# Kernel tuning notes

Hardware: AMD Instinct MI355X
Metric: run time of the kernel (lower is better)

## Reference

```python
import jax, jax.numpy as jnp
import numpy as np

K = 3        # kernel size
PAD = 1      # padding
DG = 16      # deformable groups
MAXR = 10.0  # max_residue_magnitude


def _lrelu(x):
    return jnp.where(x >= 0, x, 0.1 * x)


def _conv3(x, w, b):
    y = jax.lax.conv_general_dilated(x, w, (1, 1), 'SAME',
                                     dimension_numbers=('NCHW', 'OIHW', 'NCHW'))
    return y + b[None, :, None, None]


def _deform_conv2d(x, offset, mask, weight, bias):
    # x: [B,Cin,H,W]; offset: [B,2*DG*K*K,H,W]; mask: [B,DG*K*K,H,W]
    B, Cin, H, W = x.shape
    Cout = weight.shape[0]
    G, Cg, K2 = DG, Cin // DG, K * K
    off = offset.reshape(B, G, K2, 2, H, W)
    dy, dx = off[:, :, :, 0], off[:, :, :, 1]
    ky = jnp.repeat(jnp.arange(K), K).astype(x.dtype)   # [K2]
    kx = jnp.tile(jnp.arange(K), K).astype(x.dtype)
    hh = jnp.arange(H, dtype=x.dtype)
    ww = jnp.arange(W, dtype=x.dtype)
    # sampling positions [B,G,K2,H,W]
    py = dy + ky[None, None, :, None, None] + hh[None, None, None, :, None] - PAD
    px = dx + kx[None, None, :, None, None] + ww[None, None, None, None, :] - PAD
    y0 = jnp.floor(py)
    x0 = jnp.floor(px)
    wy1 = py - y0
    wx1 = px - x0
    xf = x.reshape(B, G, Cg, H * W)

    def gather(yi, xi, wgt):
        valid = (yi >= 0) & (yi <= H - 1) & (xi >= 0) & (xi <= W - 1)
        idx = (jnp.clip(yi, 0, H - 1).astype(jnp.int32) * W
               + jnp.clip(xi, 0, W - 1).astype(jnp.int32)).reshape(B, G, -1)
        vals = jnp.take_along_axis(
            xf, jnp.broadcast_to(idx[:, :, None, :], (B, G, Cg, idx.shape[-1])), axis=3)
        vals = vals.reshape(B, G, Cg, K2, H, W)
        w = (wgt * valid.astype(x.dtype))[:, :, None]  # [B,G,1,K2,H,W]
        return vals * w

    s = (gather(y0, x0, (1 - wy1) * (1 - wx1))
         + gather(y0, x0 + 1, (1 - wy1) * wx1)
         + gather(y0 + 1, x0, wy1 * (1 - wx1))
         + gather(y0 + 1, x0 + 1, wy1 * wx1))
    s = s * mask.reshape(B, G, K2, H, W)[:, :, None]
    wr = weight.reshape(Cout, G, Cg, K2)
    out = jnp.einsum('ogck,bgckhw->bohw', wr, s)
    return out + bias[None, :, None, None]


def setup_inputs() -> dict:
    key = jax.random.key(0)
    ks = jax.random.split(key, 16)
    B, Cin, Cout, H, W = 4, 128, 64, 96, 96
    Coff = 3 * Cout + 4  # 196
    stdv = 1.0 / np.sqrt(Cin * K * K)
    inp = {
        'x': jax.random.normal(ks[0], (B, Cin, H, W), jnp.float32),
        'extra_feat': jax.random.normal(ks[1], (B, 3 * Cout, H, W), jnp.float32),
        'flow_1': jax.random.normal(ks[2], (B, 2, H, W), jnp.float32),
        'flow_2': jax.random.normal(ks[3], (B, 2, H, W), jnp.float32),
        'weight': jax.random.uniform(ks[4], (Cout, Cin, K, K), jnp.float32, -stdv, stdv),
        'bias': jax.random.normal(ks[5], (Cout,), jnp.float32) * 0.01,
        'ow0': jax.random.normal(ks[6], (Cout, Coff, K, K), jnp.float32) * 0.02,
        'ob0': jnp.zeros((Cout,), jnp.float32),
        'ow1': jax.random.normal(ks[7], (Cout, Cout, K, K), jnp.float32) * 0.02,
        'ob1': jnp.zeros((Cout,), jnp.float32),
        'ow2': jax.random.normal(ks[8], (Cout, Cout, K, K), jnp.float32) * 0.02,
        'ob2': jnp.zeros((Cout,), jnp.float32),
        'ow3': jax.random.normal(ks[9], (27 * DG, Cout, K, K), jnp.float32) * 0.01,
        'ob3': jnp.zeros((27 * DG,), jnp.float32),
    }
    return inp


def reference(x, extra_feat, flow_1, flow_2, weight, bias,
              ow0, ob0, ow1, ob1, ow2, ob2, ow3, ob3):
    feat = jnp.concatenate([extra_feat, flow_1, flow_2], axis=1)
    h = _lrelu(_conv3(feat, ow0, ob0))
    h = _lrelu(_conv3(h, ow1, ob1))
    h = _lrelu(_conv3(h, ow2, ob2))
    out = _conv3(h, ow3, ob3)
    o1, o2, m = jnp.split(out, 3, axis=1)
    offs = MAXR * jnp.tanh(jnp.concatenate([o1, o2], axis=1))
    off1, off2 = jnp.split(offs, 2, axis=1)
    off1 = off1 + jnp.tile(flow_1[:, ::-1], (1, off1.shape[1] // 2, 1, 1))
    off2 = off2 + jnp.tile(flow_2[:, ::-1], (1, off2.shape[1] // 2, 1, 1))
    offset = jnp.concatenate([off1, off2], axis=1)
    mask = jax.nn.sigmoid(m)
    return _deform_conv2d(x, offset, mask, weight, bias)
```

## Files before the change

kernel.cpp:

```cpp
#include <hip/hip_runtime.h>
#include <math.h>

#define HW 9216
#define Hh 96
#define Ww 96
#define PHW 9604
#define QSLOTS 9604

typedef __attribute__((ext_vector_type(8))) short bh8;
typedef __attribute__((ext_vector_type(4))) short bh4;
typedef __attribute__((ext_vector_type(4))) float f32x4;
typedef __attribute__((ext_vector_type(2))) float f32x2;
typedef __attribute__((ext_vector_type(4))) int i32x4;
union bh8i { bh8 v; i32x4 i; };

__device__ __forceinline__ short f2bf(float f) {
    union { float f; unsigned u; } v; v.f = f;
    unsigned r = v.u + 0x7FFFu + ((v.u >> 16) & 1u);
    return (short)(r >> 16);
}
__device__ __forceinline__ float bf2f(short s) {
    union { unsigned u; float f; } v; v.u = ((unsigned)(unsigned short)s) << 16;
    return v.f;
}
__device__ __forceinline__ float lo_bf(unsigned u) {
    union { unsigned u; float f; } v; v.u = u << 16; return v.f;
}
__device__ __forceinline__ float hi_bf(unsigned u) {
    union { unsigned u; float f; } v; v.u = u & 0xFFFF0000u; return v.f;
}
__device__ __forceinline__ int cvt_pk_bf16(float lo, float hi) {
    int r;
    asm("v_cvt_pk_bf16_f32 %0, %1, %2" : "=v"(r) : "v"(lo), "v"(hi));
    return r;
}

__global__ void prep_misc(short* __restrict__ xpad1, short* __restrict__ hpa,
                          short* __restrict__ hpb, short* __restrict__ xdp,
                          const float* __restrict__ ow0, const float* __restrict__ ow1,
                          const float* __restrict__ ow2, const float* __restrict__ ow3,
                          const float* __restrict__ wd,
                          short* __restrict__ wb0, short* __restrict__ wb1,
                          short* __restrict__ wb2, short* __restrict__ wb3,
                          short* __restrict__ wbd) {
    int i = blockIdx.x * 256 + threadIdx.x;
    const int z1 = 4 * 388 * 224, z2 = 4 * 388 * 64;
    if (i < z1 + 2 * z2) {
        short* p; int C;
        if (i < z1) { p = xpad1; C = 224; }
        else if (i < z1 + z2) { p = hpa; C = 64; i -= z1; }
        else { p = hpb; C = 64; i -= z1 + z2; }
        int c = i % C;
        int r = i / C;
        int b = r / 388, pid = r - b * 388;
        int row, col;
        if (pid < 98)       { row = 0;  col = pid; }
        else if (pid < 196) { row = 97; col = pid - 98; }
        else if (pid < 292) { row = pid - 196 + 1; col = 0; }
        else                { row = pid - 292 + 1; col = 97; }
        p[((size_t)b * PHW + row * 98 + col) * C + c] = 0;
        return;
    }
    i -= z1 + 2 * z2;
    const int zr = 64 * 579 * 4;
    if (i < zr) {
        int piece = i & 3;
        int r2 = i >> 2;
        int s = r2 % 579, bg = r2 / 579;
        int y, x;
        if (s < 98)       { y = 0;  x = s; }
        else if (s < 196) { y = 96; x = s - 98; }
        else if (s < 294) { y = 97; x = s - 196; }
        else {
            int s2 = s - 294;
            int xi = s2 / 95;
            x = (xi == 0) ? 0 : ((xi == 1) ? 96 : 97);
            y = 1 + s2 - xi * 95;
        }
        *(bh8*)&xdp[(((size_t)bg * QSLOTS) + y * 98 + x) * 32 + piece * 8] =
            (bh8){0, 0, 0, 0, 0, 0, 0, 0};
        return;
    }
    i -= zr;
    const int n0 = 64 * 9 * 224, n1 = 64 * 9 * 64, n3 = 448 * 9 * 64, nd = 144 * 64 * 8;
    if (i < n0) {
        int co = i / (9 * 224); int r = i - co * (9 * 224);
        int tap = r / 224, ci = r - tap * 224;
        wb0[i] = f2bf(ci < 196 ? ow0[(co * 196 + ci) * 9 + tap] : 0.f);
        return;
    }
    i -= n0;
    if (i < n1) {
        int co = i / (9 * 64); int r = i - co * (9 * 64);
        int tap = r / 64, ci = r - tap * 64;
        wb1[i] = f2bf(ow1[(co * 64 + ci) * 9 + tap]);
        return;
    }
    i -= n1;
    if (i < n1) {
        int co = i / (9 * 64); int r = i - co * (9 * 64);
        int tap = r / 64, ci = r - tap * 64;
        wb2[i] = f2bf(ow2[(co * 64 + ci) * 9 + tap]);
        return;
    }
    i -= n1;
    if (i < n3) {
        int co = i / (9 * 64); int r = i - co * (9 * 64);
        int tap = r / 64, ci = r - tap * 64;
        wb3[i] = f2bf(co < 432 ? ow3[(co * 64 + ci) * 9 + tap] : 0.f);
        return;
    }
    i -= n3;
    if (i < nd) {
        int gt = i >> 9, r = i & 511;
        int co = r >> 3, c = r & 7;
        int g = gt / 9, tap = gt - g * 9;
        wbd[i] = f2bf(wd[(co * 128 + g * 8 + c) * 9 + tap]);
    }
}

__global__ void pack_all(const float* __restrict__ extra,
                         const float* __restrict__ f1,
                         const float* __restrict__ f2,
                         const float* __restrict__ x,
                         short* __restrict__ xp,
                         short* __restrict__ xdp) {
    __shared__ float t[32][33];
    const int tid = threadIdx.x, tx = tid & 31, ty = tid >> 5;
    const int pt = blockIdx.x, b = blockIdx.z;
    if (blockIdx.y < 7) {
        const int ct = blockIdx.y;
#pragma unroll
        for (int j = 0; j < 4; ++j) {
            int ch = ct * 32 + ty + j * 8;
            int p = pt * 32 + tx;
            float v = 0.f;
            if (ch < 192)      v = extra[(b * 192 + ch) * HW + p];
            else if (ch < 194) v = f1[(b * 2 + ch - 192) * HW + p];
            else if (ch < 196) v = f2[(b * 2 + ch - 194) * HW + p];
            t[ty + j * 8][tx] = v;
        }
        __syncthreads();
#pragma unroll
        for (int j = 0; j < 4; ++j) {
            int pr = ty + j * 8;
            int p = pt * 32 + pr;
            int r = p / 96, c = p - r * 96;
            xp[((size_t)b * PHW + (r + 1) * 98 + (c + 1)) * 224 + ct * 32 + tx] =
                f2bf(t[tx][pr]);
        }
    } else {
        const int ct = blockIdx.y - 7;
#pragma unroll
        for (int j = 0; j < 4; ++j) {
            int ch = ct * 32 + ty + j * 8;
            t[ty + j * 8][tx] = x[((size_t)b * 128 + ch) * HW + pt * 32 + tx];
        }
        __syncthreads();
        if (tid < 128) {
            int oct = tid >> 5, p = tid & 31;
            int g = ct * 4 + oct;
            int pix = pt * 32 + p;
            int r = pix / 96, c = pix - r * 96;
            bh8 v;
#pragma unroll
            for (int cc = 0; cc < 8; ++cc) v[cc] = f2bf(t[oct * 8 + cc][p]);
            size_t sb = ((size_t)b * 16 + g) * QSLOTS;
            int pr = r + 1, pc = c + 1;
            *(bh8*)&xdp[(sb + pr * 98 + pc) * 32 + 0]        = v;
            *(bh8*)&xdp[(sb + pr * 98 + pc - 1) * 32 + 8]    = v;
            *(bh8*)&xdp[(sb + (pr - 1) * 98 + pc) * 32 + 16] = v;
            *(bh8*)&xdp[(sb + (pr - 1) * 98 + pc - 1) * 32 + 24] = v;
        }
    }
}

template<int CINP, int KCH>
__launch_bounds__(256)
__global__ void conv_mfma(const short* __restrict__ xp,
                          const short* __restrict__ wb,
                          const float* __restrict__ bias,
                          short* __restrict__ o1) {
    __shared__ __attribute__((aligned(16))) short smA[9 * 64 * 32];
    const int tid = threadIdx.x;
    const int lane = tid & 63, wv = tid >> 6;
    const int q = lane >> 4, l15 = lane & 15;
    const int b = blockIdx.y;
    const int pix0 = blockIdx.x * 64 + wv * 16;
    const int soh = pix0 / 96, sow = pix0 - (pix0 / 96) * 96;

    const short* bp = xp + ((size_t)b * PHW + soh * 98 + sow + l15) * CINP + q * 8;

    const int sco = tid >> 2, sqq = tid & 3;
    const short* wsrc = wb + (size_t)sco * (9 * CINP) + sqq * 8;

    f32x4 acc[4];
#pragma unroll
    for (int t = 0; t < 4; ++t) acc[t] = (f32x4){0.f, 0.f, 0.f, 0.f};

    for (int p = 0; p < KCH; ++p) {
        __syncthreads();
        bh8 wtmp[9];
#pragma unroll
        for (int tap = 0; tap < 9; ++tap)
            wtmp[tap] = *(const bh8*)(wsrc + tap * CINP + p * 32);
#pragma unroll
        for (int tap = 0; tap < 9; ++tap)
            *(bh8*)&smA[tap * 2048 + sco * 32 + sqq * 8] = wtmp[tap];
        __syncthreads();
#pragma unroll
        for (int tap = 0; tap < 9; ++tap) {
            const int ky = tap / 3, kx = tap - (tap / 3) * 3;
            bh8 bf = *(const bh8*)(bp + (ky * 98 + kx) * CINP + p * 32);
#pragma unroll
            for (int t = 0; t < 4; ++t) {
                bh8 af = *(const bh8*)&smA[tap * 2048 + (t * 16 + l15) * 32 + q * 8];
                acc[t] = __builtin_amdgcn_mfma_f32_16x16x32_bf16(af, bf, acc[t], 0, 0, 0);
            }
        }
    }

    size_t base = ((size_t)b * PHW + (soh + 1) * 98 + sow + l15 + 1) * 64;
#pragma unroll
    for (int t = 0; t < 4; ++t) {
        bh4 v4;
#pragma unroll
        for (int r = 0; r < 4; ++r) {
            int co = t * 16 + q * 4 + r;
            float v = acc[t][r] + bias[co];
            v = (v >= 0.f) ? v : 0.1f * v;
            v4[r] = f2bf(v);
        }
        *(bh4*)(o1 + base + t * 16 + q * 4) = v4;
    }
}

__launch_bounds__(256)
__global__ void conv4_gemm(const short* __restrict__ xp,
                           const short* __restrict__ wb,
                           const float* __restrict__ bias,
                           float* __restrict__ offp,
                           short* __restrict__ maskb,
                           const float* __restrict__ flow1,
                           const float* __restrict__ flow2) {
    __shared__ __attribute__((aligned(16))) short smA[64 * 64];
    __shared__ __attribute__((aligned(16))) short smB[192 * 64];
    const int tid = threadIdx.x;
    const int lane = tid & 63, wv = tid >> 6;
    const int q = lane >> 4, l15 = lane & 15;
    const int pg = blockIdx.x;
    const int b = blockIdx.y;
    const int cob = blockIdx.z * 64;
    const int r0 = pg * 2;

    f32x4 acc[3][4];
#pragma unroll
    for (int pf = 0; pf < 3; ++pf)
#pragma unroll
        for (int cf = 0; cf < 4; ++cf) acc[pf][cf] = (f32x4){0.f, 0.f, 0.f, 0.f};

    for (int tap = 0; tap < 9; ++tap) {
        const int ky = tap / 3, kx = tap - (tap / 3) * 3;
        __syncthreads();
#pragma unroll
        for (int it = 0; it < 2; ++it) {
            int id = it * 256 + tid;
            int row = id >> 3, s = id & 7;
            int sw = s ^ (row & 7);
            *(bh8*)&smA[row * 64 + sw * 8] =
                *(const bh8*)(wb + (size_t)(cob + row) * 576 + tap * 64 + s * 8);
        }
#pragma unroll
        for (int it = 0; it < 6; ++it) {
            int id = it * 256 + tid;
            int row = id >> 3, s = id & 7;
            int sw = s ^ (row & 7);
            int srow = (row >= 96) ? 1 : 0;
            int scol = row - srow * 96;
            *(bh8*)&smB[row * 64 + sw * 8] = *(const bh8*)&xp[
                ((size_t)b * PHW + (r0 + srow + ky) * 98 + scol + kx) * 64 + s * 8];
        }
        __syncthreads();
#pragma unroll
        for (int kc = 0; kc < 2; ++kc) {
            bh8 bf[3], af[4];
#pragma unroll
            for (int pf = 0; pf < 3; ++pf) {
                int row = wv * 48 + pf * 16 + l15;
                int sw = (kc * 4 + q) ^ (row & 7);
                bf[pf] = *(const bh8*)&smB[row * 64 + sw * 8];
            }
#pragma unroll
            for (int cf = 0; cf < 4; ++cf) {
                int row = cf * 16 + l15;
                int sw = (kc * 4 + q) ^ (row & 7);
                af[cf] = *(const bh8*)&smA[row * 64 + sw * 8];
            }
#pragma unroll
            for (int pf = 0; pf < 3; ++pf)
#pragma unroll
                for (int cf = 0; cf < 4; ++cf)
                    acc[pf][cf] = __builtin_amdgcn_mfma_f32_16x16x32_bf16(
                        af[cf], bf[pf], acc[pf][cf], 0, 0, 0);
        }
    }

#pragma unroll
    for (int pf = 0; pf < 3; ++pf) {
        int local = wv * 48 + pf * 16 + l15;
        int lrow = (local >= 96) ? 1 : 0;
        int pix = (r0 + lrow) * 96 + (local - lrow * 96);
#pragma unroll
        for (int cf = 0; cf < 4; ++cf) {
            int cb0 = cob + cf * 16 + q * 4;
            if (cb0 < 288) {
                const float* fl = (cb0 < 144) ? flow1 : flow2;
                float fe = fl[(b * 2 + 1) * HW + pix];
                float fo = fl[(b * 2) * HW + pix];
                float t0 = 10.f * tanhf(acc[pf][cf][0] + bias[cb0 + 0]) + fe;
                float t1 = 10.f * tanhf(acc[pf][cf][1] + bias[cb0 + 1]) + fo;
                float t2 = 10.f * tanhf(acc[pf][cf][2] + bias[cb0 + 2]) + fe;
                float t3 = 10.f * tanhf(acc[pf][cf][3] + bias[cb0 + 3]) + fo;
                size_t p0 = ((size_t)b * 144 + (cb0 >> 1)) * HW + pix;
                *(f32x2*)&offp[p0 * 2] = (f32x2){t0, t1};
                *(f32x2*)&offp[(p0 + HW) * 2] = (f32x2){t2, t3};
            } else {
#pragma unroll
                for (int r = 0; r < 4; ++r) {
                    int chn = cb0 + r;
                    if (chn < 432) {
                        float v = acc[pf][cf][r] + bias[chn];
                        maskb[((size_t)b * 144 + (chn - 288)) * HW + pix] =
                            f2bf(1.f / (1.f + expf(-v)));
                    }
                }
            }
        }
    }
}

__launch_bounds__(256)
__global__ void deform_mfma(const short* __restrict__ xdp,
                            const float* __restrict__ offp,
                            const short* __restrict__ maskb,
                            const short* __restrict__ wbd,
                            const float* __restrict__ bias,
                            float* __restrict__ out) {
    __shared__ float red[4][1024];
    const int tid = threadIdx.x;
    const int lane = tid & 63, wv = tid >> 6;
    const int q = lane >> 4, l15 = lane & 15;
    const int blk = blockIdx.x;
    const int xs = blk & 7, idx = blk >> 3;
    const int b = xs >> 1;
    const int pix0 = ((xs & 1) * 288 + idx) * 16;
    const int pix = pix0 + l15;
    const int h = pix / 96, w = pix - (pix / 96) * 96;

    const short* xb = xdp + (size_t)b * 16 * QSLOTS * 32;

    f32x4 acc[4];
#pragma unroll
    for (int t = 0; t < 4; ++t) acc[t] = (f32x4){0.f, 0.f, 0.f, 0.f};

#pragma unroll
    for (int chunk = 0; chunk < 4; ++chunk) {
        const int g = wv * 4 + chunk;
        const float* opp = offp + (((size_t)b * 144 + g * 9) * HW + pix) * 2;
        const short* mp  = maskb + ((size_t)b * 144 + g * 9) * HW + pix;

        f32x2 dxy[9];
        float mk[9];
#pragma unroll
        for (int i = 0; i < 9; ++i) {
            dxy[i] = *(const f32x2*)(opp + (size_t)i * HW * 2);
            mk[i]  = bf2f(mp[(size_t)i * HW]);
        }

        int soff[9];
        float wq[9];
#pragma unroll
        for (int i = 0; i < 9; ++i) {
            float py = dxy[i][0] + (float)(i / 3) + (float)h - 1.f;
            float px = dxy[i][1] + (float)(i % 3) + (float)w - 1.f;
            py = fminf(fmaxf(py, -1.f), 96.f);
            px = fminf(fmaxf(px, -1.f), 96.f);
            float y0f = floorf(py), x0f = floorf(px);
            float wy1 = py - y0f, wx1 = px - x0f;
            int yp = (int)y0f + 1, xp = (int)x0f + 1;
            soff[i] = ((g * QSLOTS + yp * 98 + xp) << 5) + q * 8;
            float wy = (q & 2) ? wy1 : (1.f - wy1);
            float wx = (q & 1) ? wx1 : (1.f - wx1);
            wq[i] = wy * wx * mk[i];
        }

#pragma unroll
        for (int i = 0; i < 9; ++i) {
            bh8i cv;
            cv.v = *(const bh8*)(xb + soff[i]);
            const f32x2 w2 = (f32x2){wq[i], wq[i]};
            bh8i bf;
#pragma unroll
            for (int k2 = 0; k2 < 4; ++k2) {
                unsigned u = (unsigned)cv.i[k2];
                f32x2 pv = (f32x2){lo_bf(u), hi_bf(u)} * w2;
                bf.i[k2] = cvt_pk_bf16(pv[0], pv[1]);
            }
            const int gt = g * 9 + i;
            const short* ap = wbd + ((size_t)gt * 64 + l15) * 8;
#pragma unroll
            for (int t = 0; t < 4; ++t) {
                bh8 af = *(const bh8*)(ap + t * 128);
                acc[t] = __builtin_amdgcn_mfma_f32_16x16x32_bf16(af, bf.v, acc[t], 0, 0, 0);
            }
        }
    }

#pragma unroll
    for (int t = 0; t < 4; ++t)
#pragma unroll
        for (int r = 0; r < 4; ++r)
            red[wv][(t * 16 + q * 4 + r) * 16 + l15] = acc[t][r];
    __syncthreads();
    for (int e = tid; e < 1024; e += 256) {
        int co = e >> 4, pl = e & 15;
        float v = red[0][e] + red[1][e] + red[2][e] + red[3][e] + bias[co];
        out[((size_t)b * 64 + co) * HW + pix0 + pl] = v;
    }
}

extern "C" void kernel_launch(void* const* d_in, const int* in_sizes, int n_in,
                              void* d_out, int out_size, void* d_ws, size_t ws_size,
                              hipStream_t stream) {
    const float* x      = (const float*)d_in[0];
    const float* extra  = (const float*)d_in[1];
    const float* flow1  = (const float*)d_in[2];
    const float* flow2  = (const float*)d_in[3];
    const float* weight = (const float*)d_in[4];
    const float* bias   = (const float*)d_in[5];
    const float* ow0    = (const float*)d_in[6];
    const float* ob0    = (const float*)d_in[7];
    const float* ow1    = (const float*)d_in[8];
    const float* ob1    = (const float*)d_in[9];
    const float* ow2    = (const float*)d_in[10];
    const float* ob2    = (const float*)d_in[11];
    const float* ow3    = (const float*)d_in[12];
    const float* ob3    = (const float*)d_in[13];
    float* out = (float*)d_out;

    char* wsb = (char*)d_ws;
    short* xpad1 = (short*)wsb;   wsb += (size_t)4 * PHW * 224 * 2;
    short* hpa   = (short*)wsb;   wsb += (size_t)4 * PHW * 64 * 2;
    short* hpb   = (short*)wsb;   wsb += (size_t)4 * PHW * 64 * 2;
    float* offpair = (float*)wsb; wsb += (size_t)4 * 144 * HW * 2 * 4;
    short* maskbuf = (short*)wsb; wsb += (size_t)4 * 144 * HW * 2;
    short* xdp     = (short*)wsb; wsb += (size_t)4 * 16 * QSLOTS * 32 * 2 + 64;
    short* wb0     = (short*)wsb; wsb += 64 * 9 * 224 * 2;
    short* wb1     = (short*)wsb; wsb += 64 * 9 * 64 * 2;
    short* wb2     = (short*)wsb; wsb += 64 * 9 * 64 * 2;
    short* wb3     = (short*)wsb; wsb += 448 * 9 * 64 * 2;
    short* wbd     = (short*)wsb;

    const int prep_total = 546304 + 148224 + 534528;
    prep_misc<<<dim3((prep_total + 255) / 256), 256, 0, stream>>>(
        xpad1, hpa, hpb, xdp, ow0, ow1, ow2, ow3, weight,
        wb0, wb1, wb2, wb3, wbd);
    pack_all<<<dim3(288, 11, 4), 256, 0, stream>>>(extra, flow1, flow2, x, xpad1, xdp);

    conv_mfma<224, 7><<<dim3(144, 4), 256, 0, stream>>>(xpad1, wb0, ob0, hpa);
    conv_mfma<64, 2><<<dim3(144, 4), 256, 0, stream>>>(hpa, wb1, ob1, hpb);
    conv_mfma<64, 2><<<dim3(144, 4), 256, 0, stream>>>(hpb, wb2, ob2, hpa);
    conv4_gemm<<<dim3(48, 4, 7), 256, 0, stream>>>(hpa, wb3, ob3, offpair,
                                                   maskbuf, flow1, flow2);
    deform_mfma<<<dim3(2304), 256, 0, stream>>>(xdp, offpair, maskbuf, wbd, bias, out);
}
```

Measured before the change: 314.3 us.

## Restructure final offset conv to stage all-tap weights and read activations directly

The last conv (64->432 channels) now keeps all 9 taps of a 64x32 weight slice in shared memory and loads activation fragments straight from global memory per wave, instead of staging both operands per tap in LDS. Each block covers 64 pixels instead of 192, so the grid triples and there are fewer barriers per block. This cuts shared-memory traffic and synchronisation but drops activation reuse across output-channel tiles within a block, relying on cache for the repeated input reads.

Result: slower. 325.7 us (+3.6%).

```diff
diff --git a/kernel.cpp b/kernel.cpp
--- a/kernel.cpp
+++ b/kernel.cpp
@@ -236,103 +236,76 @@
 }
 
 __launch_bounds__(256)
-__global__ void conv4_gemm(const short* __restrict__ xp,
+__global__ void conv4_mfma(const short* __restrict__ xp,
                            const short* __restrict__ wb,
                            const float* __restrict__ bias,
                            float* __restrict__ offp,
                            short* __restrict__ maskb,
                            const float* __restrict__ flow1,
                            const float* __restrict__ flow2) {
-    __shared__ __attribute__((aligned(16))) short smA[64 * 64];
-    __shared__ __attribute__((aligned(16))) short smB[192 * 64];
+    __shared__ __attribute__((aligned(16))) short smA[9 * 64 * 32];
     const int tid = threadIdx.x;
     const int lane = tid & 63, wv = tid >> 6;
     const int q = lane >> 4, l15 = lane & 15;
-    const int pg = blockIdx.x;
     const int b = blockIdx.y;
     const int cob = blockIdx.z * 64;
-    const int r0 = pg * 2;
-
-    f32x4 acc[3][4];
-#pragma unroll
-    for (int pf = 0; pf < 3; ++pf)
-#pragma unroll
-        for (int cf = 0; cf < 4; ++cf) acc[pf][cf] = (f32x4){0.f, 0.f, 0.f, 0.f};
-
-    for (int tap = 0; tap < 9; ++tap) {
-        const int ky = tap / 3, kx = tap - (tap / 3) * 3;
-        __syncthreads();
-#pragma unroll
-        for (int it = 0; it < 2; ++it) {
-            int id = it * 256 + tid;
-            int row = id >> 3, s = id & 7;
-            int sw = s ^ (row & 7);
-            *(bh8*)&smA[row * 64 + sw * 8] =
-                *(const bh8*)(wb + (size_t)(cob + row) * 576 + tap * 64 + s * 8);
-        }
-#pragma unroll
-        for (int it = 0; it < 6; ++it) {
-            int id = it * 256 + tid;
-            int row = id >> 3, s = id & 7;
-            int sw = s ^ (row & 7);
-            int srow = (row >= 96) ? 1 : 0;
-            int scol = row - srow * 96;
-            *(bh8*)&smB[row * 64 + sw * 8] = *(const bh8*)&xp[
-                ((size_t)b * PHW + (r0 + srow + ky) * 98 + scol + kx) * 64 + s * 8];
-        }
-        __syncthreads();
-#pragma unroll
-        for (int kc = 0; kc < 2; ++kc) {
-            bh8 bf[3], af[4];
-#pragma unroll
-            for (int pf = 0; pf < 3; ++pf) {
-                int row = wv * 48 + pf * 16 + l15;
-                int sw = (kc * 4 + q) ^ (row & 7);
-                bf[pf] = *(const bh8*)&smB[row * 64 + sw * 8];
+    const int pix0 = blockIdx.x * 64 + wv * 16;
+    const int soh = pix0 / 96, sow = pix0 - (pix0 / 96) * 96;
+
+    const short* bp = xp + ((size_t)b * PHW + soh * 98 + sow + l15) * 64 + q * 8;
+
+    const int sco = tid >> 2, sqq = tid & 3;
+    const short* wsrc = wb + (size_t)(cob + sco) * 576 + sqq * 8;
+
+    f32x4 acc[4];
+#pragma unroll
+    for (int t = 0; t < 4; ++t) acc[t] = (f32x4){0.f, 0.f, 0.f, 0.f};
+
+    for (int p = 0; p < 2; ++p) {
+        __syncthreads();
+        bh8 wtmp[9];
+#pragma unroll
+        for (int tap = 0; tap < 9; ++tap)
+            wtmp[tap] = *(const bh8*)(wsrc + tap * 64 + p * 32);
+#pragma unroll
+        for (int tap = 0; tap < 9; ++tap)
+            *(bh8*)&smA[tap * 2048 + sco * 32 + sqq * 8] = wtmp[tap];
+        __syncthreads();
+#pragma unroll
+        for (int tap = 0; tap < 9; ++tap) {
+            const int ky = tap / 3, kx = tap - (tap / 3) * 3;
+            bh8 bf = *(const bh8*)(bp + (ky * 98 + kx) * 64 + p * 32);
+#pragma unroll
+            for (int t = 0; t < 4; ++t) {
+                bh8 af = *(const bh8*)&smA[tap * 2048 + (t * 16 + l15) * 32 + q * 8];
+                acc[t] = __builtin_amdgcn_mfma_f32_16x16x32_bf16(af, bf, acc[t], 0, 0, 0);
             }
-#pragma unroll
-            for (int cf = 0; cf < 4; ++cf) {
-                int row = cf * 16 + l15;
-                int sw = (kc * 4 + q) ^ (row & 7);
-                af[cf] = *(const bh8*)&smA[row * 64 + sw * 8];
-            }
-#pragma unroll
-            for (int pf = 0; pf < 3; ++pf)
-#pragma unroll
-                for (int cf = 0; cf < 4; ++cf)
-                    acc[pf][cf] = __builtin_amdgcn_mfma_f32_16x16x32_bf16(
-                        af[cf], bf[pf], acc[pf][cf], 0, 0, 0);
-        }
-    }
-
-#pragma unroll
-    for (int pf = 0; pf < 3; ++pf) {
-        int local = wv * 48 + pf * 16 + l15;
-        int lrow = (local >= 96) ? 1 : 0;
-        int pix = (r0 + lrow) * 96 + (local - lrow * 96);
-#pragma unroll
-        for (int cf = 0; cf < 4; ++cf) {
-            int cb0 = cob + cf * 16 + q * 4;
-            if (cb0 < 288) {
-                const float* fl = (cb0 < 144) ? flow1 : flow2;
-                float fe = fl[(b * 2 + 1) * HW + pix];
-                float fo = fl[(b * 2) * HW + pix];
-                float t0 = 10.f * tanhf(acc[pf][cf][0] + bias[cb0 + 0]) + fe;
-                float t1 = 10.f * tanhf(acc[pf][cf][1] + bias[cb0 + 1]) + fo;
-                float t2 = 10.f * tanhf(acc[pf][cf][2] + bias[cb0 + 2]) + fe;
-                float t3 = 10.f * tanhf(acc[pf][cf][3] + bias[cb0 + 3]) + fo;
-                size_t p0 = ((size_t)b * 144 + (cb0 >> 1)) * HW + pix;
-                *(f32x2*)&offp[p0 * 2] = (f32x2){t0, t1};
-                *(f32x2*)&offp[(p0 + HW) * 2] = (f32x2){t2, t3};
-            } else {
-#pragma unroll
-                for (int r = 0; r < 4; ++r) {
-                    int chn = cb0 + r;
-                    if (chn < 432) {
-                        float v = acc[pf][cf][r] + bias[chn];
-                        maskb[((size_t)b * 144 + (chn - 288)) * HW + pix] =
-                            f2bf(1.f / (1.f + expf(-v)));
-                    }
+        }
+    }
+
+    const int pix = pix0 + l15;
+#pragma unroll
+    for (int t = 0; t < 4; ++t) {
+        int cb0 = cob + t * 16 + q * 4;
+        if (cb0 < 288) {
+            const float* fl = (cb0 < 144) ? flow1 : flow2;
+            float fe = fl[(b * 2 + 1) * HW + pix];
+            float fo = fl[(b * 2) * HW + pix];
+            float t0 = 10.f * tanhf(acc[t][0] + bias[cb0 + 0]) + fe;
+            float t1 = 10.f * tanhf(acc[t][1] + bias[cb0 + 1]) + fo;
+            float t2 = 10.f * tanhf(acc[t][2] + bias[cb0 + 2]) + fe;
+            float t3 = 10.f * tanhf(acc[t][3] + bias[cb0 + 3]) + fo;
+            size_t p0 = ((size_t)b * 144 + (cb0 >> 1)) * HW + pix;
+            *(f32x2*)&offp[p0 * 2] = (f32x2){t0, t1};
+            *(f32x2*)&offp[(p0 + HW) * 2] = (f32x2){t2, t3};
+        } else {
+#pragma unroll
+            for (int r = 0; r < 4; ++r) {
+                int chn = cb0 + r;
+                if (chn < 432) {
+                    float v = acc[t][r] + bias[chn];
+                    maskb[((size_t)b * 144 + (chn - 288)) * HW + pix] =
+                        f2bf(1.f / (1.f + expf(-v)));
                 }
             }
         }
@@ -470,7 +443,7 @@
     conv_mfma<224, 7><<<dim3(144, 4), 256, 0, stream>>>(xpad1, wb0, ob0, hpa);
     conv_mfma<64, 2><<<dim3(144, 4), 256, 0, stream>>>(hpa, wb1, ob1, hpb);
     conv_mfma<64, 2><<<dim3(144, 4), 256, 0, stream>>>(hpb, wb2, ob2, hpa);
-    conv4_gemm<<<dim3(48, 4, 7), 256, 0, stream>>>(hpa, wb3, ob3, offpair,
-                                                   maskbuf, flow1, flow2);
+    conv4_mfma<<<dim3(144, 4, 7), 256, 0, stream>>>(hpa, wb3, ob3, offpair,
+                                                    maskbuf, flow1, flow2);
     deform_mfma<<<dim3(2304), 256, 0, stream>>>(xdp, offpair, maskbuf, wbd, bias, out);
 }
```
